# Kernel tuning notes

Hardware: AMD Instinct MI355X
Metric: run time of the kernel (lower is better)

Reference implementation:

```python
import jax, jax.numpy as jnp
import numpy as np

H_IMG, W_IMG = 48, 64  # feature-map resolution hard-coded in the module
NUM_HEADS = 8


def get_positional_encodings(B, N, dtype=jnp.float32):
    # (p3^2, p4^2, p3*p4, p3, p4, 1) on normalized grid; intrinsics=None path
    ys = jnp.linspace(-1.0, 1.0, H_IMG, dtype=dtype)
    xs = jnp.linspace(-1.0, 1.0, W_IMG, dtype=dtype)
    p3 = jnp.tile(ys, W_IMG)           # [N] = ys repeated W times (torch repeat)
    p4 = jnp.repeat(xs, H_IMG)         # [N] = each x repeated H times
    pos = jnp.stack([p3 * p3, p4 * p4, p3 * p4, p3, p4, jnp.ones_like(p3)], axis=-1)  # [N,6]
    return jnp.broadcast_to(pos[None], (B, N, 6))


def setup_inputs() -> dict:
    key = jax.random.key(0)
    k1, k2, k3, k4, k5 = jax.random.split(key, 5)
    B, N, C = 2, H_IMG * W_IMG, 256
    s = 0.02
    return {
        "x1": jax.random.normal(k1, (B, N, C), jnp.float32),
        "x2": jax.random.normal(k2, (B, N, C), jnp.float32),
        "Wq": jax.random.normal(k3, (C, C), jnp.float32) * s,      # qkv (one-way: q only)
        "Wkv": jax.random.normal(k4, (C, 2 * C), jnp.float32) * s,  # qkv2 -> k,v
        "Wpf": jax.random.normal(k5, (C + 6 * NUM_HEADS, C), jnp.float32) * s,  # proj_fundamental
        "bpf": jnp.zeros((C,), jnp.float32),
    }


def reference(x1, x2, Wq, Wkv, Wpf, bpf):
    B, N, C = x1.shape
    H = NUM_HEADS
    d = C // H
    scale = d ** -0.5

    # q from x1; k,v from x2 (separate linear, matching torch reshape/permute split)
    q1 = (x1 @ Wq).reshape(B, N, H, d).transpose(0, 2, 1, 3)          # [B,H,N,d]
    kv = (x2 @ Wkv).reshape(B, N, 2, H, d)
    k2 = kv[:, :, 0].transpose(0, 2, 1, 3)                            # [B,H,N,d]
    v2 = kv[:, :, 1].transpose(0, 2, 1, 3)                            # [B,H,N,d]

    attn = jax.nn.softmax(jnp.einsum('bhnd,bhmd->bhnm', q1, k2) * scale, axis=-1)  # [B,H,N,N]

    pos = get_positional_encodings(B, N, x1.dtype)                    # [B,N,6]
    v2p = jnp.concatenate(
        [v2, jnp.broadcast_to(pos[:, None], (B, H, N, 6))], axis=-1)  # [B,H,N,d+6]

    y = jnp.einsum('bhnm,bhmd->bhnd', attn, v2p)                      # [B,H,N,d+6]
    y = y.transpose(0, 2, 1, 3).reshape(B, N, H * (d + 6))            # [B,N,C+6H]
    y = y @ Wpf + bpf                                                 # [B,N,C]
    y = y.reshape(B, N, H, d).transpose(0, 2, 1, 3)                   # [B,H,N,d]

    return jnp.concatenate([attn, y], axis=-1)                        # [B,H,N,N+d]
```

## Files before the change

kernel.cpp:

```cpp
#include <hip/hip_runtime.h>
#include <hip/hip_bf16.h>
#include <cstdint>
#include <cstddef>

#define NB 2
#define NH 8
#define BHN 16
#define NN 3072
#define CC 256
#define DD 32
#define OUTW 3104
#define VW 48
#define KP 384

typedef __attribute__((ext_vector_type(8))) __bf16 bf16x8;
typedef __attribute__((ext_vector_type(4))) short short4v;
typedef __attribute__((ext_vector_type(4))) float f32x4;

static __device__ __forceinline__ unsigned short f2bf(float f) {
    __hip_bfloat16 h = __float2bfloat16(f);
    return *reinterpret_cast<unsigned short*>(&h);
}

static __device__ __forceinline__ bf16x8 ldb8(const unsigned short* p) {
    return *(const bf16x8*)p;
}

static __device__ __forceinline__ f32x4 mfma16(bf16x8 a, bf16x8 b, f32x4 c) {
    return __builtin_amdgcn_mfma_f32_16x16x32_bf16(a, b, c, 0, 0, 0);
}

static __device__ __forceinline__ float bfhi2f(unsigned u) {
    union { unsigned u; float f; } v; v.u = u & 0xffff0000u; return v.f;
}
static __device__ __forceinline__ float bflo2f(unsigned u) {
    union { unsigned u; float f; } v; v.u = u << 16; return v.f;
}

__global__ __launch_bounds__(256) void prep_kernel(
    const float* __restrict__ x1, const float* __restrict__ x2,
    const float* __restrict__ Wq, const float* __restrict__ Wkv,
    const float* __restrict__ Wpf,
    unsigned short* __restrict__ x1b, unsigned short* __restrict__ x2b,
    unsigned short* __restrict__ Wt, unsigned short* __restrict__ Wpft,
    unsigned short* __restrict__ v2pT)
{
    int i = blockIdx.x * 256 + threadIdx.x;
    const int S_X = NB * NN * CC;
    if (i < S_X) { x1b[i] = f2bf(x1[i]); return; }
    i -= S_X;
    if (i < S_X) { x2b[i] = f2bf(x2[i]); return; }
    i -= S_X;
    const int S_WT = 768 * CC;
    if (i < S_WT) {
        int j = i >> 8, kk = i & 255;
        float w = (j < 256) ? Wq[kk * 256 + j] : Wkv[kk * 512 + (j - 256)];
        Wt[i] = f2bf(w);
        return;
    }
    i -= S_WT;
    const int S_WP = 256 * KP;
    if (i < S_WP) {
        int c2 = i / KP, t = i - c2 * KP;
        int h = t / VW, cc = t - h * VW;
        unsigned short v = 0;
        if (cc < 38) v = f2bf(Wpf[(h * 38 + cc) * 256 + c2]);
        Wpft[i] = v;
        return;
    }
    i -= S_WP;
    const int S_POS = BHN * 16 * NN;
    if (i < S_POS) {
        int n = i % NN;
        int r = i / NN;
        int bh = r >> 4;
        int c = (r & 15) + 32;
        float val = 0.f;
        if (c < 38) {
            float p3 = -1.f + 2.f * (float)(n % 48) / 47.f;
            float p4 = -1.f + 2.f * (float)(n / 48) / 63.f;
            float pv[6] = { p3 * p3, p4 * p4, p3 * p4, p3, p4, 1.f };
            val = pv[c - 32];
        }
        v2pT[((size_t)bh * VW + c) * NN + n] = f2bf(val);
    }
}

__global__ __launch_bounds__(256) void qkv_kernel(
    const unsigned short* __restrict__ x1b, const unsigned short* __restrict__ x2b,
    const unsigned short* __restrict__ Wt,
    unsigned short* __restrict__ qbh, unsigned short* __restrict__ kbh,
    unsigned short* __restrict__ v2pT)
{
    int rt = blockIdx.x, ct = blockIdx.y;
    int wv = threadIdx.x >> 6, lane = threadIdx.x & 63;
    int g = lane >> 4, q = lane & 15;
    int row0 = rt * 64 + wv * 16;
    const unsigned short* A = (ct < 4) ? x1b : x2b;
    const unsigned short* arow = A + (size_t)(row0 + q) * CC + g * 8;
    const unsigned short* brow = Wt + (size_t)(ct * 64 + q) * CC + g * 8;
    f32x4 acc[4];
    #pragma unroll
    for (int cb = 0; cb < 4; ++cb) acc[cb] = f32x4{0.f, 0.f, 0.f, 0.f};
    for (int k0 = 0; k0 < CC; k0 += 32) {
        bf16x8 af = ldb8(arow + k0);
        #pragma unroll
        for (int cb = 0; cb < 4; ++cb)
            acc[cb] = mfma16(af, ldb8(brow + (size_t)cb * 16 * CC + k0), acc[cb]);
    }
    int b = row0 / NN, nb = row0 % NN;
    #pragma unroll
    for (int cb = 0; cb < 4; ++cb) {
        int jj = ct * 64 + cb * 16 + q;
        #pragma unroll
        for (int r = 0; r < 4; ++r) {
            int n = nb + 4 * g + r;
            unsigned short bv = f2bf(acc[cb][r]);
            if (jj < 256) {
                int h = jj >> 5, c = jj & 31;
                qbh[(size_t)((b * NH + h) * NN + n) * DD + c] = bv;
            } else if (jj < 512) {
                int jk = jj - 256; int h = jk >> 5, c = jk & 31;
                kbh[(size_t)((b * NH + h) * NN + n) * DD + c] = bv;
            } else {
                int jv = jj - 512; int h = jv >> 5, c = jv & 31;
                v2pT[(size_t)((b * NH + h) * VW + c) * NN + n] = bv;
            }
        }
    }
}

__global__ __launch_bounds__(256) void attn_kernel(
    const unsigned short* __restrict__ qbh, const unsigned short* __restrict__ kbh,
    const unsigned short* __restrict__ v2pT,
    float* __restrict__ out, unsigned short* __restrict__ yacc)
{
    __shared__ unsigned short tile[16][1024];
    __shared__ float lred[4][16];
    const float C = 0.17677669529663687f * 1.4426950408889634f;

    int id = blockIdx.x;
    int xcd = id & 7;
    int slot = id >> 3;
    int bh = xcd * 2 + (slot & 1);
    int tl = slot >> 1;
    int qrow = tl * 16;

    int wv = threadIdx.x >> 6, lane = threadIdx.x & 63;
    int g = lane >> 4, q = lane & 15;

    bf16x8 qf = ldb8(qbh + (size_t)(bh * NN + qrow + q) * DD + g * 8);
    const unsigned short* kbase = kbh + (size_t)bh * NN * DD;
    const unsigned short* vbase = v2pT + (size_t)bh * VW * NN;

    float l = 0.f;
    {
        int mb = wv * 768;
        bf16x8 kf0 = ldb8(kbase + (size_t)(mb + q) * DD + g * 8);
        bf16x8 kf1 = ldb8(kbase + (size_t)(mb + 16 + q) * DD + g * 8);
        for (int it = 0; it < 24; ++it) {
            int m0 = mb + it * 32;
            bf16x8 kn0 = ldb8(kbase + (size_t)(m0 + 32 + q) * DD + g * 8);
            bf16x8 kn1 = ldb8(kbase + (size_t)(m0 + 48 + q) * DD + g * 8);
            f32x4 z = {0.f, 0.f, 0.f, 0.f};
            f32x4 s0 = mfma16(kf0, qf, z);
            f32x4 s1 = mfma16(kf1, qf, z);
            #pragma unroll
            for (int r = 0; r < 4; ++r)
                l += exp2f(s0[r] * C) + exp2f(s1[r] * C);
            kf0 = kn0; kf1 = kn1;
        }
    }
    l += __shfl_xor(l, 16, 64);
    l += __shfl_xor(l, 32, 64);
    if (lane < 16) lred[wv][q] = l;
    __syncthreads();
    float nl2 = -__log2f(lred[0][q] + lred[1][q] + lred[2][q] + lred[3][q]);

    f32x4 yt0 = {0.f,0.f,0.f,0.f}, yt1 = yt0, yt2 = yt0;
    char* tbase = (char*)&tile[0][0];
    char* prowc = tbase + q * 2048;
    unsigned swq = (unsigned)((q & 7) << 4);
    int wb = wv * 512;

    for (int ph = 0; ph < 3; ++ph) {
        int pbase = ph * 1024 + wv * 256;
        bf16x8 kf0 = ldb8(kbase + (size_t)(pbase + q) * DD + g * 8);
        bf16x8 kf1 = ldb8(kbase + (size_t)(pbase + 16 + q) * DD + g * 8);
        bf16x8 vf0 = ldb8(vbase + (size_t)(q) * NN + pbase + g * 8);
        bf16x8 vf1 = ldb8(vbase + (size_t)(16 + q) * NN + pbase + g * 8);
        bf16x8 vf2 = ldb8(vbase + (size_t)(32 + q) * NN + pbase + g * 8);
        #pragma unroll
        for (int it2 = 0; it2 < 8; ++it2) {
            int m0 = pbase + it2 * 32;
            int mn = (it2 < 7) ? (m0 + 32) : ((ph + 1) * 1024 + wv * 256);
            bf16x8 kn0 = ldb8(kbase + (size_t)(mn + q) * DD + g * 8);
            bf16x8 kn1 = ldb8(kbase + (size_t)(mn + 16 + q) * DD + g * 8);
            bf16x8 vn0 = ldb8(vbase + (size_t)(q) * NN + mn + g * 8);
            bf16x8 vn1 = ldb8(vbase + (size_t)(16 + q) * NN + mn + g * 8);
            bf16x8 vn2 = ldb8(vbase + (size_t)(32 + q) * NN + mn + g * 8);

            f32x4 z = {0.f, 0.f, 0.f, 0.f};
            f32x4 s0 = mfma16(kf0, qf, z);
            f32x4 s1 = mfma16(kf1, qf, z);
            short4v pk0, pk1;
            #pragma unroll
            for (int r = 0; r < 4; ++r) {
                pk0[r] = (short)f2bf(exp2f(__builtin_fmaf(s0[r], C, nl2)));
                pk1[r] = (short)f2bf(exp2f(__builtin_fmaf(s1[r], C, nl2)));
            }
            unsigned b0 = (unsigned)(wb + it2 * 64 + 8 * g);
            *(short4v*)(prowc + (b0 ^ swq)) = pk0;
            *(short4v*)(prowc + ((b0 + 32) ^ swq)) = pk1;
            asm volatile("s_waitcnt lgkmcnt(0)" ::: "memory");
            __builtin_amdgcn_sched_barrier(0);
            bf16x8 pf = *(const bf16x8*)(prowc + ((unsigned)(wb + it2 * 64 + 16 * g) ^ swq));
            yt0 = mfma16(vf0, pf, yt0);
            yt1 = mfma16(vf1, pf, yt1);
            yt2 = mfma16(vf2, pf, yt2);
            kf0 = kn0; kf1 = kn1; vf0 = vn0; vf1 = vn1; vf2 = vn2;
        }
        __syncthreads();
        #pragma unroll
        for (int j = 0; j < 4; ++j) {
            int r = wv * 4 + j;
            const char* rsrc = tbase + r * 2048;
            unsigned swr = (unsigned)((r & 7) << 4);
            float* dst = out + (size_t)(bh * NN + qrow + r) * OUTW + ph * 1024 + lane * 4;
            #pragma unroll
            for (int st = 0; st < 4; ++st) {
                unsigned off = ((unsigned)(st * 512 + lane * 8)) ^ swr;
                unsigned long long d = *(const unsigned long long*)(rsrc + off);
                unsigned dlo = (unsigned)d, dhi = (unsigned)(d >> 32);
                f32x4 v;
                v[0] = bflo2f(dlo); v[1] = bfhi2f(dlo);
                v[2] = bflo2f(dhi); v[3] = bfhi2f(dhi);
                __builtin_nontemporal_store(v, (f32x4*)(dst + st * 256));
            }
        }
        __syncthreads();
    }

    float* yl = (float*)tbase;
    {
        f32x4 yts[3] = { yt0, yt1, yt2 };
        #pragma unroll
        for (int cb = 0; cb < 3; ++cb)
            #pragma unroll
            for (int r = 0; r < 4; ++r)
                yl[(wv * 48 + cb * 16 + 4 * g + r) * 17 + q] = yts[cb][r];
    }
    __syncthreads();
    {
        int t = threadIdx.x;
        if (t < 192) {
            int c0 = (t >> 4) << 2;
            int qq = t & 15;
            int b = bh >> 3, h = bh & 7;
            short4v pk;
            #pragma unroll
            for (int rr = 0; rr < 4; ++rr) {
                int c = c0 + rr;
                float s = yl[(0 * 48 + c) * 17 + qq] + yl[(1 * 48 + c) * 17 + qq]
                        + yl[(2 * 48 + c) * 17 + qq] + yl[(3 * 48 + c) * 17 + qq];
                pk[rr] = (short)f2bf(s);
            }
            *(short4v*)(yacc + (size_t)(b * NN + qrow + qq) * KP + h * VW + c0) = pk;
        }
    }
}

__global__ __launch_bounds__(256) void proj_kernel(
    const unsigned short* __restrict__ yacc, const unsigned short* __restrict__ Wpft,
    const float* __restrict__ bpf, float* __restrict__ out)
{
    int rt = blockIdx.x, ct = blockIdx.y;
    int wv = threadIdx.x >> 6, lane = threadIdx.x & 63;
    int g = lane >> 4, q = lane & 15;
    int row0 = rt * 64 + wv * 16;
    const unsigned short* arow = yacc + (size_t)(row0 + q) * KP + g * 8;
    const unsigned short* b0 = Wpft + (size_t)(ct * 64 + q) * KP + g * 8;
    f32x4 acc[4];
    #pragma unroll
    for (int cb = 0; cb < 4; ++cb) acc[cb] = f32x4{0.f, 0.f, 0.f, 0.f};
    for (int k0 = 0; k0 < KP; k0 += 32) {
        bf16x8 af = ldb8(arow + k0);
        #pragma unroll
        for (int cb = 0; cb < 4; ++cb)
            acc[cb] = mfma16(af, ldb8(b0 + (size_t)cb * 16 * KP + k0), acc[cb]);
    }
    int b = row0 / NN, nb = row0 % NN;
    #pragma unroll
    for (int cb = 0; cb < 4; ++cb) {
        int c2 = ct * 64 + cb * 16 + q;
        float bias = bpf[c2];
        int h = c2 >> 5, c = c2 & 31;
        float* obase = out + (size_t)((b * NH + h) * NN) * OUTW + NN + c;
        #pragma unroll
        for (int r = 0; r < 4; ++r) {
            int n = nb + 4 * g + r;
            __builtin_nontemporal_store(acc[cb][r] + bias, &obase[(size_t)n * OUTW]);
        }
    }
}

extern "C" void kernel_launch(void* const* d_in, const int* in_sizes, int n_in,
                              void* d_out, int out_size, void* d_ws, size_t ws_size,
                              hipStream_t stream)
{
    (void)in_sizes; (void)n_in; (void)out_size; (void)ws_size;
    const float* x1  = (const float*)d_in[0];
    const float* x2  = (const float*)d_in[1];
    const float* Wq  = (const float*)d_in[2];
    const float* Wkv = (const float*)d_in[3];
    const float* Wpf = (const float*)d_in[4];
    const float* bpf = (const float*)d_in[5];
    float* out = (float*)d_out;
    char* ws = (char*)d_ws;

    unsigned short* x1b  = (unsigned short*)(ws + 0);
    unsigned short* x2b  = (unsigned short*)(ws + 3145728);
    unsigned short* Wt   = (unsigned short*)(ws + 6291456);
    unsigned short* Wpft = (unsigned short*)(ws + 6684672);
    unsigned short* qbh  = (unsigned short*)(ws + 6881280);
    unsigned short* kbh  = (unsigned short*)(ws + 10027008);
    unsigned short* v2pT = (unsigned short*)(ws + 13172736);
    unsigned short* yacc = (unsigned short*)(ws + 17891328);

    prep_kernel<<<16512, 256, 0, stream>>>(x1, x2, Wq, Wkv, Wpf, x1b, x2b, Wt, Wpft, v2pT);
    qkv_kernel<<<dim3(96, 12), 256, 0, stream>>>(x1b, x2b, Wt, qbh, kbh, v2pT);
    attn_kernel<<<3072, 256, 0, stream>>>(qbh, kbh, v2pT, out, yacc);
    proj_kernel<<<dim3(96, 4), 256, 0, stream>>>(yacc, Wpft, bpf, out);
}
```

Measured before the change: 258.6 us.

## Use 8 waves per attention block with full-row P tile and single store phase

Doubles the attention block to 512 threads so each wave handles 384 keys instead of 768, and enlarges the shared tile to hold the full 3072-wide probability row so the three-phase loop with its per-phase barriers collapses into one pass followed by one store pass. The y partial reduction moves to a dedicated shared buffer summed over 8 waves, and the XCD-aware block-to-head mapping is replaced by a simple id&15 mapping. Shared memory per block grows to about 126 KB, which limits occupancy to one block per CU, and the dropped XCD mapping may reduce L2 locality for K/V.

```diff
diff --git a/kernel.cpp b/kernel.cpp
--- a/kernel.cpp
+++ b/kernel.cpp
@@ -130,24 +130,24 @@
     }
 }
 
-__global__ __launch_bounds__(256) void attn_kernel(
+__global__ __launch_bounds__(512) void attn_kernel(
     const unsigned short* __restrict__ qbh, const unsigned short* __restrict__ kbh,
     const unsigned short* __restrict__ v2pT,
     float* __restrict__ out, unsigned short* __restrict__ yacc)
 {
-    __shared__ unsigned short tile[16][1024];
-    __shared__ float lred[4][16];
+    __shared__ unsigned short tile[16][3072];
+    __shared__ float lred[8][16];
+    __shared__ float yl[8][48][17];
     const float C = 0.17677669529663687f * 1.4426950408889634f;
 
     int id = blockIdx.x;
-    int xcd = id & 7;
-    int slot = id >> 3;
-    int bh = xcd * 2 + (slot & 1);
-    int tl = slot >> 1;
+    int bh = id & 15;
+    int tl = id >> 4;
     int qrow = tl * 16;
 
     int wv = threadIdx.x >> 6, lane = threadIdx.x & 63;
     int g = lane >> 4, q = lane & 15;
+    int mb = wv * 384;
 
     bf16x8 qf = ldb8(qbh + (size_t)(bh * NN + qrow + q) * DD + g * 8);
     const unsigned short* kbase = kbh + (size_t)bh * NN * DD;
@@ -155,10 +155,9 @@
 
     float l = 0.f;
     {
-        int mb = wv * 768;
         bf16x8 kf0 = ldb8(kbase + (size_t)(mb + q) * DD + g * 8);
         bf16x8 kf1 = ldb8(kbase + (size_t)(mb + 16 + q) * DD + g * 8);
-        for (int it = 0; it < 24; ++it) {
+        for (int it = 0; it < 12; ++it) {
             int m0 = mb + it * 32;
             bf16x8 kn0 = ldb8(kbase + (size_t)(m0 + 32 + q) * DD + g * 8);
             bf16x8 kn1 = ldb8(kbase + (size_t)(m0 + 48 + q) * DD + g * 8);
@@ -175,25 +174,26 @@
     l += __shfl_xor(l, 32, 64);
     if (lane < 16) lred[wv][q] = l;
     __syncthreads();
-    float nl2 = -__log2f(lred[0][q] + lred[1][q] + lred[2][q] + lred[3][q]);
+    float lt = 0.f;
+    #pragma unroll
+    for (int w = 0; w < 8; ++w) lt += lred[w][q];
+    float nl2 = -__log2f(lt);
 
     f32x4 yt0 = {0.f,0.f,0.f,0.f}, yt1 = yt0, yt2 = yt0;
-    char* tbase = (char*)&tile[0][0];
-    char* prowc = tbase + q * 2048;
+    char* prow = (char*)&tile[0][0] + q * 6144;
     unsigned swq = (unsigned)((q & 7) << 4);
-    int wb = wv * 512;
-
-    for (int ph = 0; ph < 3; ++ph) {
-        int pbase = ph * 1024 + wv * 256;
-        bf16x8 kf0 = ldb8(kbase + (size_t)(pbase + q) * DD + g * 8);
-        bf16x8 kf1 = ldb8(kbase + (size_t)(pbase + 16 + q) * DD + g * 8);
-        bf16x8 vf0 = ldb8(vbase + (size_t)(q) * NN + pbase + g * 8);
-        bf16x8 vf1 = ldb8(vbase + (size_t)(16 + q) * NN + pbase + g * 8);
-        bf16x8 vf2 = ldb8(vbase + (size_t)(32 + q) * NN + pbase + g * 8);
-        #pragma unroll
-        for (int it2 = 0; it2 < 8; ++it2) {
-            int m0 = pbase + it2 * 32;
-            int mn = (it2 < 7) ? (m0 + 32) : ((ph + 1) * 1024 + wv * 256);
+    int wb = wv * 768;
+
+    {
+        bf16x8 kf0 = ldb8(kbase + (size_t)(mb + q) * DD + g * 8);
+        bf16x8 kf1 = ldb8(kbase + (size_t)(mb + 16 + q) * DD + g * 8);
+        bf16x8 vf0 = ldb8(vbase + (size_t)(q) * NN + mb + g * 8);
+        bf16x8 vf1 = ldb8(vbase + (size_t)(16 + q) * NN + mb + g * 8);
+        bf16x8 vf2 = ldb8(vbase + (size_t)(32 + q) * NN + mb + g * 8);
+        #pragma unroll 4
+        for (int it2 = 0; it2 < 12; ++it2) {
+            int m0 = mb + it2 * 32;
+            int mn = m0 + 32;
             bf16x8 kn0 = ldb8(kbase + (size_t)(mn + q) * DD + g * 8);
             bf16x8 kn1 = ldb8(kbase + (size_t)(mn + 16 + q) * DD + g * 8);
             bf16x8 vn0 = ldb8(vbase + (size_t)(q) * NN + mn + g * 8);
@@ -210,47 +210,46 @@
                 pk1[r] = (short)f2bf(exp2f(__builtin_fmaf(s1[r], C, nl2)));
             }
             unsigned b0 = (unsigned)(wb + it2 * 64 + 8 * g);
-            *(short4v*)(prowc + (b0 ^ swq)) = pk0;
-            *(short4v*)(prowc + ((b0 + 32) ^ swq)) = pk1;
+            *(short4v*)(prow + (b0 ^ swq)) = pk0;
+            *(short4v*)(prow + ((b0 + 32) ^ swq)) = pk1;
             asm volatile("s_waitcnt lgkmcnt(0)" ::: "memory");
             __builtin_amdgcn_sched_barrier(0);
-            bf16x8 pf = *(const bf16x8*)(prowc + ((unsigned)(wb + it2 * 64 + 16 * g) ^ swq));
+            bf16x8 pf = *(const bf16x8*)(prow + ((unsigned)(wb + it2 * 64 + 16 * g) ^ swq));
             yt0 = mfma16(vf0, pf, yt0);
             yt1 = mfma16(vf1, pf, yt1);
             yt2 = mfma16(vf2, pf, yt2);
             kf0 = kn0; kf1 = kn1; vf0 = vn0; vf1 = vn1; vf2 = vn2;
         }
-        __syncthreads();
-        #pragma unroll
-        for (int j = 0; j < 4; ++j) {
-            int r = wv * 4 + j;
-            const char* rsrc = tbase + r * 2048;
-            unsigned swr = (unsigned)((r & 7) << 4);
-            float* dst = out + (size_t)(bh * NN + qrow + r) * OUTW + ph * 1024 + lane * 4;
-            #pragma unroll
-            for (int st = 0; st < 4; ++st) {
-                unsigned off = ((unsigned)(st * 512 + lane * 8)) ^ swr;
-                unsigned long long d = *(const unsigned long long*)(rsrc + off);
-                unsigned dlo = (unsigned)d, dhi = (unsigned)(d >> 32);
-                f32x4 v;
-                v[0] = bflo2f(dlo); v[1] = bfhi2f(dlo);
-                v[2] = bflo2f(dhi); v[3] = bfhi2f(dhi);
-                __builtin_nontemporal_store(v, (f32x4*)(dst + st * 256));
-            }
-        }
-        __syncthreads();
-    }
-
-    float* yl = (float*)tbase;
+    }
+    __syncthreads();
+
+    #pragma unroll
+    for (int j = 0; j < 2; ++j) {
+        int r = wv * 2 + j;
+        const char* rsrc = (const char*)&tile[0][0] + r * 6144;
+        unsigned swr = (unsigned)((r & 7) << 4);
+        float* dst = out + (size_t)(bh * NN + qrow + r) * OUTW + lane * 4;
+        #pragma unroll
+        for (int c = 0; c < 12; ++c) {
+            unsigned off = ((unsigned)(c * 512 + lane * 8)) ^ swr;
+            unsigned long long d = *(const unsigned long long*)(rsrc + off);
+            unsigned dlo = (unsigned)d, dhi = (unsigned)(d >> 32);
+            f32x4 v;
+            v[0] = bflo2f(dlo); v[1] = bfhi2f(dlo);
+            v[2] = bflo2f(dhi); v[3] = bfhi2f(dhi);
+            __builtin_nontemporal_store(v, (f32x4*)(dst + c * 256));
+        }
+    }
+
     {
         f32x4 yts[3] = { yt0, yt1, yt2 };
         #pragma unroll
         for (int cb = 0; cb < 3; ++cb)
             #pragma unroll
             for (int r = 0; r < 4; ++r)
-                yl[(wv * 48 + cb * 16 + 4 * g + r) * 17 + q] = yts[cb][r];
-    }
-    __syncthreads();
+                yl[wv][cb * 16 + 4 * g + r][q] = yts[cb][r];
+    }
+    asm volatile("s_waitcnt lgkmcnt(0)\n\ts_barrier" ::: "memory");
     {
         int t = threadIdx.x;
         if (t < 192) {
@@ -261,8 +260,9 @@
             #pragma unroll
             for (int rr = 0; rr < 4; ++rr) {
                 int c = c0 + rr;
-                float s = yl[(0 * 48 + c) * 17 + qq] + yl[(1 * 48 + c) * 17 + qq]
-                        + yl[(2 * 48 + c) * 17 + qq] + yl[(3 * 48 + c) * 17 + qq];
+                float s = 0.f;
+                #pragma unroll
+                for (int w = 0; w < 8; ++w) s += yl[w][c][qq];
                 pk[rr] = (short)f2bf(s);
             }
             *(short4v*)(yacc + (size_t)(b * NN + qrow + qq) * KP + h * VW + c0) = pk;
@@ -329,6 +329,6 @@
 
     prep_kernel<<<16512, 256, 0, stream>>>(x1, x2, Wq, Wkv, Wpf, x1b, x2b, Wt, Wpft, v2pT);
     qkv_kernel<<<dim3(96, 12), 256, 0, stream>>>(x1b, x2b, Wt, qbh, kbh, v2pT);
-    attn_kernel<<<3072, 256, 0, stream>>>(qbh, kbh, v2pT, out, yacc);
+    attn_kernel<<<3072, 512, 0, stream>>>(qbh, kbh, v2pT, out, yacc);
     proj_kernel<<<dim3(96, 4), 256, 0, stream>>>(yacc, Wpft, bpf, out);
 }
```

Result: slower. 298.9 us (+15.6%).
